# Kernel tuning notes

Hardware: AMD Instinct MI355X
Metric: run time of the kernel (lower is better)

## Reference

```python
import jax, jax.numpy as jnp
import numpy as np

DIM = 1024; HEADS = 8; DHEAD = 64; INNER = HEADS * DHEAD
WS = 512; B = 2; N = 2048; FF = 4 * DIM
NEG = -1e9


def layernorm(x, g, b, eps=1e-5):
    mu = jnp.mean(x, -1, keepdims=True)
    var = jnp.mean((x - mu) ** 2, -1, keepdims=True)
    return (x - mu) * jax.lax.rsqrt(var + eps) * g + b


def rmsnorm(x, g, eps=1e-6):
    return x * jax.lax.rsqrt(jnp.mean(x * x, -1, keepdims=True) + eps) * g


def rotate_half(x):
    x1, x2 = jnp.split(x, 2, -1)
    return jnp.concatenate([-x2, x1], -1)


def local_attention(q, k, v):
    # lucidrains LocalAttention: single-head over last dim, rotary pos emb,
    # window_size=WS, causal, look_backward=1, look_forward=0. n % WS == 0 so autopad no-op.
    b, n, d = q.shape
    w = n // WS
    inv_freq = 1.0 / (10000.0 ** (jnp.arange(0, d, 2, dtype=jnp.float32) / d))
    t = jnp.arange(n)
    freqs = t[:, None].astype(jnp.float32) * inv_freq[None, :]
    emb = jnp.concatenate([freqs, freqs], -1)           # [n, d]
    cos, sin = jnp.cos(emb), jnp.sin(emb)
    q = q * cos + rotate_half(q) * sin
    k = k * cos + rotate_half(k) * sin
    bq = q.reshape(b, w, WS, d) * (d ** -0.5)
    bk = k.reshape(b, w, WS, d)
    bv = v.reshape(b, w, WS, d)

    def look_around(x, pad_value):
        # gather current window + 1 window backward along the window axis
        pads = [(0, 0), (1, 0)] + [(0, 0)] * (x.ndim - 2)
        xp = jnp.pad(x, pads, constant_values=pad_value)
        return jnp.concatenate([xp[:, 0:w], xp[:, 1:w + 1]], axis=2)

    bk = look_around(bk, 0.0)                 # [b, w, 2*WS, d]
    bv = look_around(bv, 0.0)
    bt = t.reshape(w, WS)                     # query positions per window
    bqk = look_around(bt[None], -1)[0]        # key positions, pad = -1  [w, 2*WS]
    sim = jnp.einsum('bwie,bwje->bwij', bq, bk)  # [b, w, WS, 2*WS]
    mask = (bt[:, :, None] < bqk[:, None, :]) | (bqk[:, None, :] == -1)
    sim = jnp.where(mask[None], NEG, sim)
    attn = jax.nn.softmax(sim, -1)
    out = jnp.einsum('bwij,bwje->bwie', attn, bv)
    return out.reshape(b, n, d)


def setup_inputs() -> dict:
    key = jax.random.key(0)
    ks = jax.random.split(key, 10)
    s = 0.02
    f32 = jnp.float32
    return {
        'text': jax.random.normal(ks[0], (B, N, DIM), f32),
        'audio': jax.random.normal(ks[1], (B, N, DIM), f32),
        'video': jax.random.normal(ks[2], (B, N, DIM), f32),
        'Wa': jax.random.normal(ks[3], (DIM, DIM), f32) * s,
        'ba': jnp.zeros((DIM,), f32),
        'lna_g': jnp.ones((DIM,), f32), 'lna_b': jnp.zeros((DIM,), f32),
        'Wvid': jax.random.normal(ks[4], (DIM, DIM), f32) * s,
        'bvid': jnp.zeros((DIM,), f32),
        'lnv_g': jnp.ones((DIM,), f32), 'lnv_b': jnp.zeros((DIM,), f32),
        'ln1_g': jnp.ones((DIM,), f32), 'ln1_b': jnp.zeros((DIM,), f32),
        'Wq': jax.random.normal(ks[5], (DIM, INNER), f32) * s,
        'Wkv': jax.random.normal(ks[6], (DIM, 2 * INNER), f32) * s,
        'qn_g': jnp.ones((DHEAD,), f32), 'kn_g': jnp.ones((DHEAD,), f32),
        'Wo': jax.random.normal(ks[7], (INNER, DIM), f32) * s,
        'W1': jax.random.normal(ks[8], (DIM, FF), f32) * s,
        'b1': jnp.zeros((FF,), f32),
        'ln2_g': jnp.ones((FF,), f32), 'ln2_b': jnp.zeros((FF,), f32),
        'W2': jax.random.normal(ks[9], (FF, DIM), f32) * s,
        'b2': jnp.zeros((DIM,), f32),
    }


def reference(text, audio, video, Wa, ba, lna_g, lna_b, Wvid, bvid, lnv_g, lnv_b,
              ln1_g, ln1_b, Wq, Wkv, qn_g, kn_g, Wo, W1, b1, ln2_g, ln2_b, W2, b2):
    # modality -> text-token adapters (audio_to_text / video_to_text): linear + layernorm
    audio_t = layernorm(audio @ Wa + ba, lna_g, lna_b)
    video_t = layernorm(video @ Wvid + bvid, lnv_g, lnv_b)
    # windowed local attention: q=text, k=audio tokens, v=video tokens
    x = local_attention(text, audio_t, video_t)          # [B, N, DIM]
    # qk-norm full causal attention (flash=False: dense [B,H,N,N] scores)
    b, n, _ = x.shape
    h = layernorm(x, ln1_g, ln1_b)
    q = (h @ Wq).reshape(b, n, HEADS, DHEAD).transpose(0, 2, 1, 3)
    k, v = jnp.split(h @ Wkv, 2, -1)
    k = k.reshape(b, n, HEADS, DHEAD).transpose(0, 2, 1, 3)
    v = v.reshape(b, n, HEADS, DHEAD).transpose(0, 2, 1, 3)
    q = rmsnorm(q, qn_g)
    k = rmsnorm(k, kn_g)
    sim = jnp.einsum('bhid,bhjd->bhij', q, k) * (DHEAD ** -0.5)
    causal = jnp.tril(jnp.ones((n, n), bool))
    sim = jnp.where(causal[None, None], sim, NEG)
    attn = jax.nn.softmax(sim, -1)
    o = jnp.einsum('bhij,bhjd->bhid', attn, v).transpose(0, 2, 1, 3).reshape(b, n, INNER)
    x = o @ Wo
    x = x + x                                            # x = x + x in source
    # FFN: Linear -> GELU -> post-act LayerNorm -> Linear, + residual
    h1 = layernorm(jax.nn.gelu(x @ W1 + b1), ln2_g, ln2_b)
    return h1 @ W2 + b2 + x
```

## Files before the change

### kernel.cpp

```cpp
#include <hip/hip_runtime.h>
#include <hip/hip_bf16.h>

typedef __bf16 bf16;
typedef __bf16 bf16x8 __attribute__((ext_vector_type(8)));
typedef float  f32x4  __attribute__((ext_vector_type(4)));

static __device__ __forceinline__ float b2f(bf16 x) { return (float)x; }
static __device__ __forceinline__ bf16  f2b(float x) { return (bf16)x; }
static __device__ __forceinline__ float ldval(float v) { return v; }
static __device__ __forceinline__ float ldval(bf16 v)  { return (float)v; }

static __device__ __forceinline__ void gl_lds16(const bf16* g, bf16* l)
{
    __builtin_amdgcn_global_load_lds(
        (const __attribute__((address_space(1))) void*)g,
        (__attribute__((address_space(3))) void*)l,
        16, 0, 0);
}

__global__ void detect_dtype(const unsigned short* __restrict__ p, int* __restrict__ flag)
{
    if (threadIdx.x == 0 && blockIdx.x == 0) {
        int big = 0;
        for (int i = 0; i < 512; ++i) {
            int e = (p[i] >> 7) & 0xFF;
            if (e >= 0xE0) big++;
        }
        *flag = (big > 0) ? 1 : 0;
    }
}

__global__ __launch_bounds__(256) void convert2(
    const void* __restrict__ sa, const void* __restrict__ sb,
    bf16* __restrict__ da, bf16* __restrict__ db, int n,
    const int* __restrict__ flag)
{
    int f = *flag;
    int half = gridDim.x >> 1;
    const void* s = (blockIdx.x < half) ? sa : sb;
    bf16* d = (blockIdx.x < half) ? da : db;
    int bid = (blockIdx.x < half) ? blockIdx.x : blockIdx.x - half;
    for (int i = bid * 256 + threadIdx.x; i < n; i += half * 256) {
        float v = f ? ((const float*)s)[i] : (float)((const bf16*)s)[i];
        d[i] = f2b(v);
    }
}

struct VecPack { const void* src[14]; int n[14]; };
__global__ __launch_bounds__(256) void convert_vecs(
    VecPack vp, bf16* __restrict__ dst, const int* __restrict__ flag)
{
    int v = blockIdx.x;
    int f = *flag;
    const void* s = vp.src[v];
    int n = vp.n[v];
    bf16* d = dst + (size_t)v * 4096;
    for (int i = threadIdx.x; i < n; i += 256) {
        float x = f ? ((const float*)s)[i] : (float)((const bf16*)s)[i];
        d[i] = f2b(x);
    }
}

template <int EPI, int MT>
__global__ __launch_bounds__(256) void gemm_bt(
    const bf16* __restrict__ A0, int lda, int zsA, int zsA2,
    const bf16* __restrict__ B0, int ldb, int zsB, int zsB2,
    void* __restrict__ C0, int ldc, int zsC, int zsC2,
    const bf16* __restrict__ bias, int zsBias, float scale, int K)
{
    constexpr int IFR = MT / 32;
    __shared__ __align__(16) bf16 As[MT * 64];
    __shared__ __align__(16) bf16 Bs[128 * 64];
    const int z = blockIdx.z;
    const bf16* A  = A0 + (size_t)z * zsA + (size_t)(z >> 2) * zsA2;
    const bf16* Bt = B0 + (size_t)z * zsB + (size_t)(z >> 2) * zsB2;
    const size_t cbase = (size_t)z * zsC + (size_t)(z >> 2) * zsC2;
    if (bias) bias += (size_t)z * zsBias;
    const int tid  = threadIdx.x;
    const int lane = tid & 63, wave = tid >> 6;
    const int quad = lane >> 4, l16 = lane & 15;
    const size_t tm = (size_t)blockIdx.y * MT, tn = (size_t)blockIdx.x * 128;
    const int wm = (wave >> 1) * (MT / 2), wn = (wave & 1) * 64;
    const int srow = lane >> 3;
    const int scol = ((lane & 7) ^ srow) * 8;

    f32x4 acc[IFR][4];
    const f32x4 zro = {0.f, 0.f, 0.f, 0.f};
    #pragma unroll
    for (int i = 0; i < IFR; ++i)
        #pragma unroll
        for (int j = 0; j < 4; ++j) acc[i][j] = zro;

    const int swzA = l16 & 7;
    for (int k0 = 0; k0 < K; k0 += 64) {
        #pragma unroll
        for (int i = 0; i < IFR; ++i) {
            int chunk = (wave * IFR + i) * 64;
            int row = (chunk >> 3) + srow;
            gl_lds16(A + (tm + row) * (size_t)lda + k0 + scol, As + (size_t)chunk * 8);
        }
        #pragma unroll
        for (int i = 0; i < 4; ++i) {
            int chunk = (wave * 4 + i) * 64;
            int row = (chunk >> 3) + srow;
            gl_lds16(Bt + (tn + row) * (size_t)ldb + k0 + scol, Bs + (size_t)chunk * 8);
        }
        __syncthreads();
        #pragma unroll
        for (int kk = 0; kk < 2; ++kk) {
            bf16x8 af[IFR], bfr[4];
            #pragma unroll
            for (int i = 0; i < IFR; ++i) {
                int row = wm + i * 16 + l16;
                af[i] = *(const bf16x8*)(const void*)&As[(row * 8 + ((kk*4 + quad) ^ swzA)) * 8];
            }
            #pragma unroll
            for (int j = 0; j < 4; ++j) {
                int row = wn + j * 16 + l16;
                bfr[j] = *(const bf16x8*)(const void*)&Bs[(row * 8 + ((kk*4 + quad) ^ swzA)) * 8];
            }
            #pragma unroll
            for (int i = 0; i < IFR; ++i)
                #pragma unroll
                for (int j = 0; j < 4; ++j)
                    acc[i][j] = __builtin_amdgcn_mfma_f32_16x16x32_bf16(
                        af[i], bfr[j], acc[i][j], 0, 0, 0);
        }
        __syncthreads();
    }

    float* Cf = (float*)C0;
    bf16*  Cb = (bf16*)C0;
    #pragma unroll
    for (int i = 0; i < IFR; ++i) {
        #pragma unroll
        for (int j = 0; j < 4; ++j) {
            size_t col = tn + wn + j*16 + l16;
            float bb = bias ? b2f(bias[col]) : 0.f;
            #pragma unroll
            for (int r = 0; r < 4; ++r) {
                size_t row = tm + wm + i*16 + quad*4 + r;
                float v = acc[i][j][r] + bb;
                size_t off = cbase + row * (size_t)ldc + col;
                if (EPI == 0) {
                    Cf[off] = v;
                } else if (EPI == 1) {
                    Cb[off] = f2b(v * scale);
                } else {
                    float g = 0.5f * v * (1.f + tanhf(0.7978845608028654f *
                                  (v + 0.044715f * v * v * v)));
                    Cb[off] = f2b(g);
                }
            }
        }
    }
}

__global__ __launch_bounds__(512, 2) void gemm_ff1_8ph(
    const bf16* __restrict__ A, int lda,
    const bf16* __restrict__ Bt, int ldb,
    bf16* __restrict__ C, int ldc,
    const bf16* __restrict__ bias, int K)
{
    __shared__ __align__(16) bf16 As[2][256 * 64];
    __shared__ __align__(16) bf16 Bs[2][256 * 64];
    const int tid  = threadIdx.x;
    const int lane = tid & 63, wave = tid >> 6;
    const int quad = lane >> 4, l16 = lane & 15;
    const int wr = wave >> 2, wc = wave & 3;
    const size_t tm = (size_t)blockIdx.y * 256;
    const size_t tn = (size_t)blockIdx.x * 256;
    const int srow = lane >> 3;
    const int scol = ((lane & 7) ^ srow) * 8;
    const int swz  = l16 & 7;

    f32x4 acc[8][4];
    const f32x4 zro = {0.f, 0.f, 0.f, 0.f};
    #pragma unroll
    for (int m = 0; m < 8; ++m)
        #pragma unroll
        for (int n = 0; n < 4; ++n) acc[m][n] = zro;

    const bf16* aSrc[4];
    const bf16* bSrc[4];
    #pragma unroll
    for (int i = 0; i < 4; ++i) {
        int grow = wave * 32 + i * 8 + srow;
        aSrc[i] = A  + (tm + grow) * (size_t)lda + scol;
        bSrc[i] = Bt + (tn + grow) * (size_t)ldb + scol;
    }

#define STAGE(BUF, K0, I)                                                     \
    do {                                                                      \
        gl_lds16(aSrc[I] + (K0), &As[BUF][(wave * 4 + (I)) * 512]);           \
        gl_lds16(bSrc[I] + (K0), &Bs[BUF][(wave * 4 + (I)) * 512]);           \
    } while (0)

#define LDA_F(BUF, M, KK)                                                     \
    (*(const bf16x8*)(const void*)&As[BUF][(wr * 128 + (M) * 16 + l16) * 64 + \
        ((((KK) * 4 + quad) ^ swz) << 3)])
#define LDB_F(BUF, N, KK)                                                     \
    (*(const bf16x8*)(const void*)&Bs[BUF][(wc * 64 + (N) * 16 + l16) * 64 +  \
        ((((KK) * 4 + quad) ^ swz) << 3)])

#define PHASE(M0, M1, PREF_STMT, TAIL_STMT)                                   \
    {                                                                         \
        PREF_STMT;                                                            \
        bf16x8 x0 = LDA_F(cur, M0, 0), x1 = LDA_F(cur, M0, 1);                \
        bf16x8 y0 = LDA_F(cur, M1, 0), y1 = LDA_F(cur, M1, 1);                \
        asm volatile("s_barrier" ::: "memory");                               \
        __builtin_amdgcn_s_setprio(1);                                        \
        _Pragma("unroll")                                                     \
        for (int n = 0; n < 4; ++n) {                                         \
            acc[M0][n] = __builtin_amdgcn_mfma_f32_16x16x32_bf16(x0, bfr[n][0], acc[M0][n], 0, 0, 0); \
            acc[M0][n] = __builtin_amdgcn_mfma_f32_16x16x32_bf16(x1, bfr[n][1], acc[M0][n], 0, 0, 0); \
            acc[M1][n] = __builtin_amdgcn_mfma_f32_16x16x32_bf16(y0, bfr[n][0], acc[M1][n], 0, 0, 0); \
            acc[M1][n] = __builtin_amdgcn_mfma_f32_16x16x32_bf16(y1, bfr[n][1], acc[M1][n], 0, 0, 0); \
        }                                                                     \
        __builtin_amdgcn_s_setprio(0);                                        \
        TAIL_STMT;                                                            \
        asm volatile("s_barrier" ::: "memory");                               \
    }

    #pragma unroll
    for (int i = 0; i < 4; ++i) STAGE(0, 0, i);
    asm volatile("s_waitcnt vmcnt(0)" ::: "memory");
    asm volatile("s_barrier" ::: "memory");

    const int NT = K >> 6;
    bf16x8 bfr[4][2];
    for (int t = 0; t < NT; ++t) {
        const int cur = t & 1, nxt = cur ^ 1;
        const int k1  = (t + 1) << 6;
        const bool pref = (t + 1 < NT);

        #pragma unroll
        for (int n = 0; n < 4; ++n) {
            bfr[n][0] = LDB_F(cur, n, 0);
            bfr[n][1] = LDB_F(cur, n, 1);
        }
        PHASE(0, 1,
              if (pref) { STAGE(nxt, k1, 0); STAGE(nxt, k1, 1); }, )
        PHASE(2, 3,
              if (pref) { STAGE(nxt, k1, 2); STAGE(nxt, k1, 3); }, )
        PHASE(4, 5, , )
        PHASE(6, 7, ,
              asm volatile("s_waitcnt vmcnt(0)" ::: "memory"))
    }
#undef PHASE
#undef LDB_F
#undef LDA_F
#undef STAGE

    #pragma unroll
    for (int m = 0; m < 8; ++m) {
        #pragma unroll
        for (int n = 0; n < 4; ++n) {
            size_t col = tn + wc * 64 + n * 16 + l16;
            float bb = b2f(bias[col]);
            #pragma unroll
            for (int r = 0; r < 4; ++r) {
                size_t row = tm + wr * 128 + m * 16 + quad * 4 + r;
                float v = acc[m][n][r] + bb;
                float s = v * (1.5957691216057308f + 0.07135481627f * v * v);
                float g = v / (1.f + __expf(-s));
                C[row * (size_t)ldc + col] = f2b(g);
            }
        }
    }
}

__global__ void transpose_any(const void* __restrict__ in, int R, int C,
                              unsigned short* __restrict__ out, int ldo,
                              const int* __restrict__ flag)
{
    __shared__ unsigned short t[32][33];
    int f = *flag;
    int c0 = blockIdx.x * 32, r0 = blockIdx.y * 32;
    int tx = threadIdx.x, ty = threadIdx.y;
    for (int i = ty; i < 32; i += 8) {
        size_t idx = (size_t)(r0 + i) * C + c0 + tx;
        bf16 v = f ? f2b(((const float*)in)[idx]) : ((const bf16*)in)[idx];
        t[i][tx] = *(unsigned short*)&v;
    }
    __syncthreads();
    for (int i = ty; i < 32; i += 8)
        out[(size_t)(c0 + i) * ldo + r0 + tx] = t[tx][i];
}

__global__ void transpose_vt(const unsigned short* __restrict__ in,
                             unsigned short* __restrict__ out)
{
    __shared__ unsigned short t[32][33];
    int b = blockIdx.z;
    const unsigned short* src = in + (size_t)b * 2048 * 1024;
    unsigned short* dst = out + (size_t)b * 1024 * 2560;
    int c0 = blockIdx.x * 32, r0 = blockIdx.y * 32;
    int tx = threadIdx.x, ty = threadIdx.y;
    for (int i = ty; i < 32; i += 8)
        t[i][tx] = src[(size_t)(r0 + i) * 1024 + c0 + tx];
    __syncthreads();
    for (int i = ty; i < 32; i += 8)
        dst[(size_t)(c0 + i) * 2560 + 512 + r0 + tx] = t[tx][i];
}

__global__ void transpose_v(const float* __restrict__ qkv, bf16* __restrict__ Vt)
{
    __shared__ float t[32][33];
    int bh = blockIdx.z, b = bh >> 3, h = bh & 7;
    const float* src = qkv + (size_t)b * 2048 * 1536 + 1024 + h * 64;
    int c0 = blockIdx.x * 32, r0 = blockIdx.y * 32;
    int tx = threadIdx.x, ty = threadIdx.y;
    for (int i = ty; i < 32; i += 8)
        t[i][tx] = src[(size_t)(r0 + i) * 1536 + c0 + tx];
    __syncthreads();
    bf16* dst = Vt + (size_t)bh * 64 * 2048;
    for (int i = ty; i < 32; i += 8)
        dst[(size_t)(c0 + i) * 2048 + r0 + tx] = f2b(t[tx][i]);
}

template <typename Tin>
__global__ __launch_bounds__(256) void ln_rows(
    const Tin* __restrict__ in, int C,
    const bf16* __restrict__ g, const bf16* __restrict__ b,
    bf16* __restrict__ out, float eps)
{
    const int row = blockIdx.x, tid = threadIdx.x;
    const Tin* p = in + (size_t)row * C;
    float s = 0.f, ss = 0.f;
    for (int c = tid; c < C; c += 256) {
        float v = ldval(p[c]);
        s += v; ss += v * v;
    }
    #pragma unroll
    for (int d = 32; d > 0; d >>= 1) { s += __shfl_xor(s, d); ss += __shfl_xor(ss, d); }
    __shared__ float red[2][4];
    int wave = tid >> 6, lane = tid & 63;
    if (lane == 0) { red[0][wave] = s; red[1][wave] = ss; }
    __syncthreads();
    s  = red[0][0] + red[0][1] + red[0][2] + red[0][3];
    ss = red[1][0] + red[1][1] + red[1][2] + red[1][3];
    float mu   = s / C;
    float var  = ss / C - mu * mu;
    float rstd = rsqrtf(var + eps);
    bf16* q = out + (size_t)row * C;
    for (int c = tid; c < C; c += 256) {
        float v = ldval(p[c]);
        q[c] = f2b((v - mu) * rstd * b2f(g[c]) + b2f(b[c]));
    }
}

__global__ __launch_bounds__(256) void ln_rows2(
    const bf16* __restrict__ in,
    const bf16* __restrict__ g0, const bf16* __restrict__ b0,
    const bf16* __restrict__ g1, const bf16* __restrict__ b1,
    bf16* __restrict__ out0, bf16* __restrict__ out1)
{
    const int row = blockIdx.x, tid = threadIdx.x;
    const int sel = row >> 12;
    const bf16* p = in + (size_t)row * 1024;
    const bf16* g = sel ? g1 : g0;
    const bf16* b = sel ? b1 : b0;
    bf16* q = (sel ? out1 + (size_t)(row - 4096) * 1024 : out0 + (size_t)row * 1024);
    float s = 0.f, ss = 0.f;
    for (int c = tid; c < 1024; c += 256) {
        float v = b2f(p[c]);
        s += v; ss += v * v;
    }
    #pragma unroll
    for (int d = 32; d > 0; d >>= 1) { s += __shfl_xor(s, d); ss += __shfl_xor(ss, d); }
    __shared__ float red[2][4];
    int wave = tid >> 6, lane = tid & 63;
    if (lane == 0) { red[0][wave] = s; red[1][wave] = ss; }
    __syncthreads();
    s  = red[0][0] + red[0][1] + red[0][2] + red[0][3];
    ss = red[1][0] + red[1][1] + red[1][2] + red[1][3];
    float mu   = s * (1.f / 1024.f);
    float var  = ss * (1.f / 1024.f) - mu * mu;
    float rstd = rsqrtf(var + 1e-5f);
    for (int c = tid; c < 1024; c += 256) {
        float v = b2f(p[c]);
        q[c] = f2b((v - mu) * rstd * b2f(g[c]) + b2f(b[c]));
    }
}

__global__ __launch_bounds__(256) void rotary_kernel(
    const void* __restrict__ text, const int* __restrict__ flag,
    const bf16* __restrict__ audioT,
    bf16* __restrict__ qrot, bf16* __restrict__ krotPad)
{
    int row = blockIdx.x;
    int t = row & 2047, b = row >> 11;
    int tid = threadIdx.x;
    int f = *flag;
    const float lg = 9.210340371976184f / 512.f;
    size_t base = (size_t)row * 1024;
    size_t kb = ((size_t)(b * 2560 + 512 + t)) * 1024;
    for (int c = tid; c < 512; c += 256) {
        float invf = __expf(-(float)c * lg);
        float th = (float)t * invf;
        float sn, cs;
        sincosf(th, &sn, &cs);
        float q1 = f ? ((const float*)text)[base + c]
                     : b2f(((const bf16*)text)[base + c]);
        float q2 = f ? ((const float*)text)[base + c + 512]
                     : b2f(((const bf16*)text)[base + c + 512]);
        qrot[base + c]       = f2b((q1 * cs - q2 * sn) * 0.03125f);
        qrot[base + c + 512] = f2b((q2 * cs + q1 * sn) * 0.03125f);
        float k1 = b2f(audioT[base + c]), k2 = b2f(audioT[base + c + 512]);
        krotPad[kb + c]       = f2b(k1 * cs - k2 * sn);
        krotPad[kb + c + 512] = f2b(k2 * cs + k1 * sn);
    }
}

__global__ __launch_bounds__(256) void softmax_local(
    const float* __restrict__ sim, bf16* __restrict__ attn)
{
    int i  = blockIdx.x;
    int zz = blockIdx.y;
    int w  = zz & 3;
    int tid = threadIdx.x;
    const float* p = sim + ((size_t)zz * 512 + i) * 1024;
    bf16* q = attn + ((size_t)zz * 512 + i) * 1024;
    int jlo = (w == 0) ? 512 : 0;
    int jhi = 512 + i;
    float m = -1e30f;
    #pragma unroll
    for (int k = 0; k < 4; ++k) {
        int c = tid + k * 256;
        if (c >= jlo && c <= jhi) m = fmaxf(m, p[c]);
    }
    #pragma unroll
    for (int d = 32; d > 0; d >>= 1) m = fmaxf(m, __shfl_xor(m, d));
    __shared__ float red[2][4];
    int wave = tid >> 6, lane = tid & 63;
    if (lane == 0) red[0][wave] = m;
    __syncthreads();
    m = fmaxf(fmaxf(red[0][0], red[0][1]), fmaxf(red[0][2], red[0][3]));
    float pv[4];
    float s = 0.f;
    #pragma unroll
    for (int k = 0; k < 4; ++k) {
        int c = tid + k * 256;
        float e = (c >= jlo && c <= jhi) ? __expf(p[c] - m) : 0.f;
        pv[k] = e; s += e;
    }
    #pragma unroll
    for (int d = 32; d > 0; d >>= 1) s += __shfl_xor(s, d);
    if (lane == 0) red[1][wave] = s;
    __syncthreads();
    s = red[1][0] + red[1][1] + red[1][2] + red[1][3];
    float inv = 1.f / s;
    #pragma unroll
    for (int k = 0; k < 4; ++k) q[tid + k * 256] = f2b(pv[k] * inv);
}

__global__ __launch_bounds__(256) void pack_qk(
    const float* __restrict__ qkv, bf16* __restrict__ Qp, bf16* __restrict__ Kp,
    const bf16* __restrict__ qn_g, const bf16* __restrict__ kn_g)
{
    int gid  = blockIdx.x * 4 + (threadIdx.x >> 6);
    int lane = threadIdx.x & 63;
    int token = gid >> 4, r = gid & 15, part = r >> 3, h = r & 7;
    const float* p = qkv + (size_t)token * 1536 + part * 512 + h * 64 + lane;
    float v = *p;
    float ss = v * v;
    #pragma unroll
    for (int d = 32; d > 0; d >>= 1) ss += __shfl_xor(ss, d);
    float sc = rsqrtf(ss * (1.f / 64.f) + 1e-6f);
    const bf16* gw = part ? kn_g : qn_g;
    float outv = v * sc * b2f(gw[lane]);
    if (!part) outv *= 0.125f;
    int b = token >> 11, t = token & 2047;
    bf16* dst = (part ? Kp : Qp) + ((size_t)(b * 8 + h) * 2048 + t) * 64 + lane;
    *dst = f2b(outv);
}

__global__ __launch_bounds__(256) void flash_split(
    const bf16* __restrict__ Qp, const bf16* __restrict__ Kp,
    const bf16* __restrict__ Vt, bf16* __restrict__ o,
    float* __restrict__ Opart, float* __restrict__ MLpart)
{
    const int qb = blockIdx.x;
    const int chunk = blockIdx.y;
    const int nch = (qb >> 3) + 1;
    if (chunk >= nch) return;
    __shared__ __align__(16) bf16 Ks[64][72];
    __shared__ __align__(16) bf16 Vs[64][72];
    __shared__ __align__(16) bf16 Ps[4][16][72];
    const int bh = blockIdx.z, b = bh >> 3, h = bh & 7;
    const int qm = qb * 64;
    const int jt0 = chunk * 512;
    const int jt1 = min(jt0 + 512, qm + 64);
    const int tid = threadIdx.x, wave = tid >> 6, lane = tid & 63;
    const int quad = lane >> 4, l16 = lane & 15;
    const bf16* Qg = Qp + (size_t)bh * 2048 * 64;
    const bf16* Kg = Kp + (size_t)bh * 2048 * 64;
    const bf16* Vg = Vt + (size_t)bh * 64 * 2048;

    const int qrow = qm + wave * 16 + l16;
    bf16x8 qa[2];
    qa[0] = *(const bf16x8*)(const void*)(Qg + (size_t)qrow * 64 + quad * 8);
    qa[1] = *(const bf16x8*)(const void*)(Qg + (size_t)qrow * 64 + 32 + quad * 8);

    f32x4 oacc[4];
    const f32x4 zro = {0.f, 0.f, 0.f, 0.f};
    #pragma unroll
    for (int j = 0; j < 4; ++j) oacc[j] = zro;
    float mst[4] = {-1e30f, -1e30f, -1e30f, -1e30f};
    float lst[4] = {0.f, 0.f, 0.f, 0.f};

    const int ldr = tid >> 2, ldc = (tid & 3) * 16;
    for (int jt = jt0; jt < jt1; jt += 64) {
        *(uint4*)(void*)&Ks[ldr][ldc] =
            *(const uint4*)(const void*)(Kg + (size_t)(jt + ldr) * 64 + ldc);
        *(uint4*)(void*)&Ks[ldr][ldc + 8] =
            *(const uint4*)(const void*)(Kg + (size_t)(jt + ldr) * 64 + ldc + 8);
        *(uint4*)(void*)&Vs[ldr][ldc] =
            *(const uint4*)(const void*)(Vg + (size_t)ldr * 2048 + jt + ldc);
        *(uint4*)(void*)&Vs[ldr][ldc + 8] =
            *(const uint4*)(const void*)(Vg + (size_t)ldr * 2048 + jt + ldc + 8);
        __syncthreads();

        f32x4 s[4];
        #pragma unroll
        for (int j = 0; j < 4; ++j) s[j] = zro;
        #pragma unroll
        for (int kk = 0; kk < 2; ++kk) {
            #pragma unroll
            for (int j = 0; j < 4; ++j) {
                bf16x8 kb = *(const bf16x8*)(const void*)&Ks[j*16 + l16][kk*32 + quad*8];
                s[j] = __builtin_amdgcn_mfma_f32_16x16x32_bf16(qa[kk], kb, s[j], 0, 0, 0);
            }
        }

        if (jt + 63 > qm + wave * 16) {
            #pragma unroll
            for (int j = 0; j < 4; ++j) {
                int key = jt + j * 16 + l16;
                #pragma unroll
                for (int r = 0; r < 4; ++r) {
                    int row = qm + wave * 16 + quad * 4 + r;
                    if (key > row) s[j][r] = -1e30f;
                }
            }
        }

        f32x4 tmax = s[0];
        #pragma unroll
        for (int j = 1; j < 4; ++j)
            #pragma unroll
            for (int r = 0; r < 4; ++r) tmax[r] = fmaxf(tmax[r], s[j][r]);
        #pragma unroll
        for (int r = 0; r < 4; ++r) {
            float tv = tmax[r];
            #pragma unroll
            for (int d = 1; d < 16; d <<= 1) tv = fmaxf(tv, __shfl_xor(tv, d));
            tmax[r] = tv;
        }
        float scl[4];
        #pragma unroll
        for (int r = 0; r < 4; ++r) {
            float mn = fmaxf(mst[r], tmax[r]);
            scl[r] = __expf(mst[r] - mn);
            mst[r] = mn;
        }
        f32x4 psum = zro;
        #pragma unroll
        for (int j = 0; j < 4; ++j)
            #pragma unroll
            for (int r = 0; r < 4; ++r) {
                float e = __expf(s[j][r] - mst[r]);
                s[j][r] = e;
                psum[r] += e;
            }
        #pragma unroll
        for (int r = 0; r < 4; ++r) {
            float tv = psum[r];
            #pragma unroll
            for (int d = 1; d < 16; d <<= 1) tv += __shfl_xor(tv, d);
            lst[r] = lst[r] * scl[r] + tv;
        }
        #pragma unroll
        for (int j = 0; j < 4; ++j)
            #pragma unroll
            for (int r = 0; r < 4; ++r) oacc[j][r] *= scl[r];

        #pragma unroll
        for (int j = 0; j < 4; ++j)
            #pragma unroll
            for (int r = 0; r < 4; ++r)
                Ps[wave][quad*4 + r][j*16 + l16] = f2b(s[j][r]);
        bf16x8 pa[2];
        pa[0] = *(const bf16x8*)(const void*)&Ps[wave][l16][quad*8];
        pa[1] = *(const bf16x8*)(const void*)&Ps[wave][l16][32 + quad*8];

        #pragma unroll
        for (int kk = 0; kk < 2; ++kk) {
            #pragma unroll
            for (int j = 0; j < 4; ++j) {
                bf16x8 vb = *(const bf16x8*)(const void*)&Vs[j*16 + l16][kk*32 + quad*8];
                oacc[j] = __builtin_amdgcn_mfma_f32_16x16x32_bf16(pa[kk], vb, oacc[j], 0, 0, 0);
            }
        }
        __syncthreads();
    }

    if (nch == 1) {
        #pragma unroll
        for (int j = 0; j < 4; ++j) {
            #pragma unroll
            for (int r = 0; r < 4; ++r) {
                int t = qm + wave * 16 + quad * 4 + r;
                o[((size_t)(b * 2048 + t)) * 512 + h * 64 + j * 16 + l16] =
                    f2b(oacc[j][r] / lst[r]);
            }
        }
    } else {
        int pidx = (bh * 32 + qb) * 4 + chunk;
        float* Od = Opart + (size_t)pidx * 4096;
        #pragma unroll
        for (int j = 0; j < 4; ++j)
            #pragma unroll
            for (int r = 0; r < 4; ++r) {
                int row = wave * 16 + quad * 4 + r;
                Od[row * 64 + j * 16 + l16] = oacc[j][r];
            }
        if (l16 == 0) {
            #pragma unroll
            for (int r = 0; r < 4; ++r) {
                int row = wave * 16 + quad * 4 + r;
                MLpart[(size_t)pidx * 128 + row]      = mst[r];
                MLpart[(size_t)pidx * 128 + 64 + row] = lst[r];
            }
        }
    }
}

__global__ __launch_bounds__(256) void flash_combine(
    const float* __restrict__ Opart, const float* __restrict__ MLpart,
    bf16* __restrict__ o)
{
    int qb = blockIdx.x + 8;
    int bh = blockIdx.y, b = bh >> 3, h = bh & 7;
    int nch = (qb >> 3) + 1;
    int row = threadIdx.x >> 2;
    int d0 = (threadIdx.x & 3) * 16;
    int base = (bh * 32 + qb) * 4;
    float m[4], l[4], w[4];
    float mstar = -1e30f;
    for (int c = 0; c < nch; ++c) {
        m[c] = MLpart[(size_t)(base + c) * 128 + row];
        l[c] = MLpart[(size_t)(base + c) * 128 + 64 + row];
        mstar = fmaxf(mstar, m[c]);
    }
    float lstar = 0.f;
    for (int c = 0; c < nch; ++c) {
        w[c] = __expf(m[c] - mstar);
        lstar += l[c] * w[c];
    }
    float inv = 1.f / lstar;
    int t = qb * 64 + row;
    bf16* op = o + ((size_t)(b * 2048 + t)) * 512 + h * 64 + d0;
    #pragma unroll 4
    for (int dd = 0; dd < 16; ++dd) {
        float acc = 0.f;
        for (int c = 0; c < nch; ++c)
            acc += Opart[(size_t)(base + c) * 4096 + row * 64 + d0 + dd] * w[c];
        op[dd] = f2b(acc * inv);
    }
}

__global__ __launch_bounds__(256) void combine_ff2(
    const float* __restrict__ p0, const float* __restrict__ p1,
    const bf16* __restrict__ x2, const bf16* __restrict__ b2,
    float* __restrict__ out)
{
    int i4 = (blockIdx.x * 256 + threadIdx.x) * 4;
    #pragma unroll
    for (int k = 0; k < 4; ++k) {
        int i = i4 + k;
        out[i] = p0[i] + p1[i] + b2f(x2[i]) + b2f(b2[i & 1023]);
    }
}

static void launch_gemm(int epi, hipStream_t s,
                        const bf16* A, int lda, int zsA, int zsA2,
                        const bf16* Bt, int ldb, int zsB, int zsB2,
                        void* C, int ldc, int zsC, int zsC2,
                        const bf16* bias, int zsBias, float scale,
                        int M, int N, int K, int nz)
{
    bool mt64 = ((M >> 7) * (N >> 7) * nz) <= 512;
    dim3 blk(256);
    if (mt64) {
        dim3 g(N / 128, M / 64, nz);
        switch (epi) {
        case 0: gemm_bt<0,64><<<g, blk, 0, s>>>(A, lda, zsA, zsA2, Bt, ldb, zsB, zsB2, C, ldc, zsC, zsC2, bias, zsBias, scale, K); break;
        case 1: gemm_bt<1,64><<<g, blk, 0, s>>>(A, lda, zsA, zsA2, Bt, ldb, zsB, zsB2, C, ldc, zsC, zsC2, bias, zsBias, scale, K); break;
        default: gemm_bt<2,64><<<g, blk, 0, s>>>(A, lda, zsA, zsA2, Bt, ldb, zsB, zsB2, C, ldc, zsC, zsC2, bias, zsBias, scale, K); break;
        }
    } else {
        dim3 g(N / 128, M / 128, nz);
        switch (epi) {
        case 0: gemm_bt<0,128><<<g, blk, 0, s>>>(A, lda, zsA, zsA2, Bt, ldb, zsB, zsB2, C, ldc, zsC, zsC2, bias, zsBias, scale, K); break;
        case 1: gemm_bt<1,128><<<g, blk, 0, s>>>(A, lda, zsA, zsA2, Bt, ldb, zsB, zsB2, C, ldc, zsC, zsC2, bias, zsBias, scale, K); break;
        default: gemm_bt<2,128><<<g, blk, 0, s>>>(A, lda, zsA, zsA2, Bt, ldb, zsB, zsB2, C, ldc, zsC, zsC2, bias, zsBias, scale, K); break;
        }
    }
}

extern "C" void kernel_launch(void* const* d_in, const int* in_sizes, int n_in,
                              void* d_out, int out_size, void* d_ws, size_t ws_size,
                              hipStream_t stream)
{
    const void* text  = d_in[0];
    const void* audio = d_in[1];
    const void* video = d_in[2];
    const void* Wa    = d_in[3];
    const void* ba    = d_in[4];
    const void* lna_g = d_in[5];
    const void* lna_b = d_in[6];
    const void* Wvid  = d_in[7];
    const void* bvid  = d_in[8];
    const void* lnv_g = d_in[9];
    const void* lnv_b = d_in[10];
    const void* ln1_g = d_in[11];
    const void* ln1_b = d_in[12];
    const void* Wq    = d_in[13];
    const void* Wkv   = d_in[14];
    const void* qn_g  = d_in[15];
    const void* kn_g  = d_in[16];
    const void* Wo    = d_in[17];
    const void* W1    = d_in[18];
    const void* b1    = d_in[19];
    const void* ln2_g = d_in[20];
    const void* ln2_b = d_in[21];
    const void* W2    = d_in[22];
    const void* b2    = d_in[23];

    char* ws = (char*)d_ws;
    size_t off = 0;
    auto alloc = [&](size_t bytes) -> char* {
        char* p = ws + off;
        off += (bytes + 255) & ~(size_t)255;
        return p;
    };
    const size_t MB = 1024 * 1024;
    int*  flag  = (int*)alloc(256);
    bf16* vecs  = (bf16*)alloc(14 * 4096 * 2);
    bf16* WqkvT = (bf16*)alloc((size_t)1536 * 1024 * 2);
    bf16* WoT   = (bf16*)alloc((size_t)1024 * 512 * 2);
    bf16* W1T   = (bf16*)alloc((size_t)4096 * 1024 * 2);
    bf16* W2T   = (bf16*)alloc((size_t)1024 * 4096 * 2);
    char* regionIn = alloc(24 * MB);
    char* region2  = alloc(32 * MB);
    char* regionH  = alloc(8 * MB);
    char* regionX  = alloc(8 * MB);
    char* regionO  = alloc(4 * MB);
    bf16* qrot    = (bf16*)alloc((size_t)4096 * 1024 * 2);
    bf16* krotPad = (bf16*)alloc((size_t)2 * 2560 * 1024 * 2);
    bf16* VTpad   = (bf16*)alloc((size_t)2 * 1024 * 2560 * 2);
    bf16* attn    = (bf16*)alloc((size_t)8 * 512 * 1024 * 2);

    bf16*  audioC = (bf16*)regionIn;
    bf16*  videoC = audioC + (size_t)4096 * 1024;
    float* qkvF   = (float*)regionIn;
    bf16*  tmp2   = (bf16*)region2;
    float* tmpF   = (float*)region2;
    float* xF     = (float*)(region2 + 16 * MB);
    bf16*  g      = (bf16*)region2;
    bf16*  audioT = (bf16*)regionH;
    bf16*  h      = (bf16*)regionH;
    bf16*  videoT = (bf16*)regionX;
    bf16*  x2     = (bf16*)regionX;
    bf16*  WaT    = (bf16*)regionO;
    bf16*  WvT    = WaT + (size_t)1024 * 1024;
    bf16*  o      = (bf16*)regionO;
    bf16*  Qp     = qrot;
    bf16*  Kp     = krotPad;
    bf16*  Vth    = attn;
    float* Opart  = (float*)regionIn;
    float* MLpart = Opart + (size_t)16 * 32 * 4 * 4096;
    float* p0     = (float*)regionIn;
    float* p1     = (float*)VTpad;

    bf16* baC   = vecs + 0 * 4096;
    bf16* bvidC = vecs + 1 * 4096;
    bf16* lnagC = vecs + 2 * 4096;
    bf16* lnabC = vecs + 3 * 4096;
    bf16* lnvgC = vecs + 4 * 4096;
    bf16* lnvbC = vecs + 5 * 4096;
    bf16* ln1gC = vecs + 6 * 4096;
    bf16* ln1bC = vecs + 7 * 4096;
    bf16* qngC  = vecs + 8 * 4096;
    bf16* kngC  = vecs + 9 * 4096;
    bf16* b1C   = vecs + 10 * 4096;
    bf16* ln2gC = vecs + 11 * 4096;
    bf16* ln2bC = vecs + 12 * 4096;
    bf16* b2C   = vecs + 13 * 4096;

    detect_dtype<<<1, 64, 0, stream>>>((const unsigned short*)text, flag);

    const int NTOK = 4096 * 1024;
    convert2<<<4096, 256, 0, stream>>>(audio, video, audioC, videoC, NTOK, flag);
    VecPack vp;
    const void* vsrc[14] = {ba, bvid, lna_g, lna_b, lnv_g, lnv_b, ln1_g, ln1_b,
                            qn_g, kn_g, b1, ln2_g, ln2_b, b2};
    int vn[14] = {1024, 1024, 1024, 1024, 1024, 1024, 1024, 1024,
                  64, 64, 4096, 4096, 4096, 1024};
    for (int i = 0; i < 14; ++i) { vp.src[i] = vsrc[i]; vp.n[i] = vn[i]; }
    convert_vecs<<<14, 256, 0, stream>>>(vp, vecs, flag);

    dim3 tb(32, 8);
    transpose_any<<<dim3(32, 32), tb, 0, stream>>>(Wa, 1024, 1024, (unsigned short*)WaT, 1024, flag);
    transpose_any<<<dim3(32, 32), tb, 0, stream>>>(Wvid, 1024, 1024, (unsigned short*)WvT, 1024, flag);
    transpose_any<<<dim3(16, 32), tb, 0, stream>>>(Wq, 1024, 512, (unsigned short*)WqkvT, 1024, flag);
    transpose_any<<<dim3(32, 32), tb, 0, stream>>>(Wkv, 1024, 1024, (unsigned short*)(WqkvT + (size_t)512 * 1024), 1024, flag);
    transpose_any<<<dim3(32, 16), tb, 0, stream>>>(Wo, 512, 1024, (unsigned short*)WoT, 512, flag);
    transpose_any<<<dim3(128, 32), tb, 0, stream>>>(W1, 1024, 4096, (unsigned short*)W1T, 1024, flag);
    transpose_any<<<dim3(32, 128), tb, 0, stream>>>(W2, 4096, 1024, (unsigned short*)W2T, 4096, flag);

    launch_gemm(1, stream, audioC, 1024, 4096*1024, 0, WaT, 1024, 1024*1024, 0,
                tmp2, 1024, 4096*1024, 0, baC, 4096, 1.f, 4096, 1024, 1024, 2);
    ln_rows2<<<8192, 256, 0, stream>>>(tmp2, lnagC, lnabC, lnvgC, lnvbC, audioT, videoT);

    hipMemsetAsync(krotPad, 0, (size_t)2 * 2560 * 1024 * 2, stream);
    hipMemsetAsync(VTpad, 0, (size_t)2 * 1024 * 2560 * 2, stream);
    rotary_kernel<<<4096, 256, 0, stream>>>(text, flag, audioT, qrot, krotPad);
    transpose_vt<<<dim3(32, 64, 2), tb, 0, stream>>>(
        (const unsigned short*)videoT, (unsigned short*)VTpad);

    launch_gemm(0, stream, qrot, 1024, 512*1024, 0,
                krotPad, 1024, 512*1024, 512*1024,
                tmpF, 1024, 512*1024, 0, nullptr, 0, 1.f, 512, 1024, 1024, 8);
    softmax_local<<<dim3(512, 8), 256, 0, stream>>>(tmpF, attn);
    launch_gemm(0, stream, attn, 1024, 512*1024, 0,
                VTpad, 2560, 512, 1024*2560 - 2048,
                xF, 1024, 512*1024, 0, nullptr, 0, 1.f, 512, 1024, 1024, 8);

    ln_rows<float><<<4096, 256, 0, stream>>>(xF, 1024, ln1gC, ln1bC, h, 1e-5f);
    launch_gemm(0, stream, h, 1024, 0, 0, WqkvT, 1024, 0, 0,
                qkvF, 1536, 0, 0, nullptr, 0, 1.f, 4096, 1536, 1024, 1);
    pack_qk<<<16384, 256, 0, stream>>>(qkvF, Qp, Kp, qngC, kngC);
    transpose_v<<<dim3(2, 64, 16), tb, 0, stream>>>(qkvF, Vth);
    flash_split<<<dim3(32, 4, 16), 256, 0, stream>>>(Qp, Kp, Vth, o, Opart, MLpart);
    flash_combine<<<dim3(24, 16), 256, 0, stream>>>(Opart, MLpart, o);

    launch_gemm(1, stream, o, 512, 0, 0, WoT, 512, 0, 0,
                x2, 1024, 0, 0, nullptr, 0, 2.f, 4096, 1024, 512, 1);
    gemm_ff1_8ph<<<dim3(16, 16), 512, 0, stream>>>(x2, 1024, W1T, 1024,
                                                   g, 4096, b1C, 1024);
    ln_rows<bf16><<<4096, 256, 0, stream>>>(g, 4096, ln2gC, ln2bC, g, 1e-5f);
    launch_gemm(0, stream, g, 4096, 2048, 0, W2T, 4096, 2048, 0,
                p0, 1024, (int)(p1 - p0), 0, nullptr, 0, 1.f, 4096, 1024, 2048, 2);
    combine_ff2<<<4096, 256, 0, stream>>>(p0, p1, x2, b2C, (float*)d_out);

    (void)in_sizes; (void)n_in; (void)out_size; (void)ws_size;
}
```

Baseline: 612.7 us.

## Fuse split-KV flash attention into single pass with double-buffered K/V prefetch

Replaces the split-KV flash attention plus combine kernel with one kernel per query block that walks all causal key tiles. Global loads for the next K/V tile are issued into registers before the current tile's MFMAs and stored into a second LDS buffer, so there is one barrier per tile. Heaviest query blocks are scheduled first. This removes the partial-output traffic and the extra combine launch, but drops parallelism to 512 blocks with a long causal tail, and doubles LDS use per block.

```diff
diff --git a/kernel.cpp b/kernel.cpp
--- a/kernel.cpp
+++ b/kernel.cpp
@@ -476,22 +476,16 @@
     *dst = f2b(outv);
 }
 
-__global__ __launch_bounds__(256) void flash_split(
+__global__ __launch_bounds__(256) void flash_fused(
     const bf16* __restrict__ Qp, const bf16* __restrict__ Kp,
-    const bf16* __restrict__ Vt, bf16* __restrict__ o,
-    float* __restrict__ Opart, float* __restrict__ MLpart)
-{
-    const int qb = blockIdx.x;
-    const int chunk = blockIdx.y;
-    const int nch = (qb >> 3) + 1;
-    if (chunk >= nch) return;
-    __shared__ __align__(16) bf16 Ks[64][72];
-    __shared__ __align__(16) bf16 Vs[64][72];
+    const bf16* __restrict__ Vt, bf16* __restrict__ o)
+{
+    __shared__ __align__(16) bf16 Ks[2][64][72];
+    __shared__ __align__(16) bf16 Vs[2][64][72];
     __shared__ __align__(16) bf16 Ps[4][16][72];
-    const int bh = blockIdx.z, b = bh >> 3, h = bh & 7;
+    const int qb = 31 - blockIdx.x;
+    const int bh = blockIdx.y, b = bh >> 3, h = bh & 7;
     const int qm = qb * 64;
-    const int jt0 = chunk * 512;
-    const int jt1 = min(jt0 + 512, qm + 64);
     const int tid = threadIdx.x, wave = tid >> 6, lane = tid & 63;
     const int quad = lane >> 4, l16 = lane & 15;
     const bf16* Qg = Qp + (size_t)bh * 2048 * 64;
@@ -511,16 +505,31 @@
     float lst[4] = {0.f, 0.f, 0.f, 0.f};
 
     const int ldr = tid >> 2, ldc = (tid & 3) * 16;
-    for (int jt = jt0; jt < jt1; jt += 64) {
-        *(uint4*)(void*)&Ks[ldr][ldc] =
-            *(const uint4*)(const void*)(Kg + (size_t)(jt + ldr) * 64 + ldc);
-        *(uint4*)(void*)&Ks[ldr][ldc + 8] =
-            *(const uint4*)(const void*)(Kg + (size_t)(jt + ldr) * 64 + ldc + 8);
-        *(uint4*)(void*)&Vs[ldr][ldc] =
-            *(const uint4*)(const void*)(Vg + (size_t)ldr * 2048 + jt + ldc);
-        *(uint4*)(void*)&Vs[ldr][ldc + 8] =
-            *(const uint4*)(const void*)(Vg + (size_t)ldr * 2048 + jt + ldc + 8);
-        __syncthreads();
+    {
+        uint4 ka = *(const uint4*)(const void*)(Kg + (size_t)ldr * 64 + ldc);
+        uint4 kb = *(const uint4*)(const void*)(Kg + (size_t)ldr * 64 + ldc + 8);
+        uint4 va = *(const uint4*)(const void*)(Vg + (size_t)ldr * 2048 + ldc);
+        uint4 vb = *(const uint4*)(const void*)(Vg + (size_t)ldr * 2048 + ldc + 8);
+        *(uint4*)(void*)&Ks[0][ldr][ldc]     = ka;
+        *(uint4*)(void*)&Ks[0][ldr][ldc + 8] = kb;
+        *(uint4*)(void*)&Vs[0][ldr][ldc]     = va;
+        *(uint4*)(void*)&Vs[0][ldr][ldc + 8] = vb;
+    }
+    __syncthreads();
+
+    const int ntiles = qb + 1;
+    for (int t = 0; t < ntiles; ++t) {
+        const int cur = t & 1, nxt = cur ^ 1;
+        const int jt = t * 64;
+        const bool pref = (t + 1 < ntiles);
+        uint4 ka, kb, va, vb;
+        if (pref) {
+            int jn = jt + 64;
+            ka = *(const uint4*)(const void*)(Kg + (size_t)(jn + ldr) * 64 + ldc);
+            kb = *(const uint4*)(const void*)(Kg + (size_t)(jn + ldr) * 64 + ldc + 8);
+            va = *(const uint4*)(const void*)(Vg + (size_t)ldr * 2048 + jn + ldc);
+            vb = *(const uint4*)(const void*)(Vg + (size_t)ldr * 2048 + jn + ldc + 8);
+        }
 
         f32x4 s[4];
         #pragma unroll
@@ -529,8 +538,8 @@
         for (int kk = 0; kk < 2; ++kk) {
             #pragma unroll
             for (int j = 0; j < 4; ++j) {
-                bf16x8 kb = *(const bf16x8*)(const void*)&Ks[j*16 + l16][kk*32 + quad*8];
-                s[j] = __builtin_amdgcn_mfma_f32_16x16x32_bf16(qa[kk], kb, s[j], 0, 0, 0);
+                bf16x8 kf = *(const bf16x8*)(const void*)&Ks[cur][j*16 + l16][kk*32 + quad*8];
+                s[j] = __builtin_amdgcn_mfma_f32_16x16x32_bf16(qa[kk], kf, s[j], 0, 0, 0);
             }
         }
 
@@ -599,75 +608,28 @@
         for (int kk = 0; kk < 2; ++kk) {
             #pragma unroll
             for (int j = 0; j < 4; ++j) {
-                bf16x8 vb = *(const bf16x8*)(const void*)&Vs[j*16 + l16][kk*32 + quad*8];
-                oacc[j] = __builtin_amdgcn_mfma_f32_16x16x32_bf16(pa[kk], vb, oacc[j], 0, 0, 0);
+                bf16x8 vf = *(const bf16x8*)(const void*)&Vs[cur][j*16 + l16][kk*32 + quad*8];
+                oacc[j] = __builtin_amdgcn_mfma_f32_16x16x32_bf16(pa[kk], vf, oacc[j], 0, 0, 0);
             }
         }
-        __syncthreads();
-    }
-
-    if (nch == 1) {
-        #pragma unroll
-        for (int j = 0; j < 4; ++j) {
-            #pragma unroll
-            for (int r = 0; r < 4; ++r) {
-                int t = qm + wave * 16 + quad * 4 + r;
-                o[((size_t)(b * 2048 + t)) * 512 + h * 64 + j * 16 + l16] =
-                    f2b(oacc[j][r] / lst[r]);
-            }
-        }
-    } else {
-        int pidx = (bh * 32 + qb) * 4 + chunk;
-        float* Od = Opart + (size_t)pidx * 4096;
-        #pragma unroll
-        for (int j = 0; j < 4; ++j)
-            #pragma unroll
-            for (int r = 0; r < 4; ++r) {
-                int row = wave * 16 + quad * 4 + r;
-                Od[row * 64 + j * 16 + l16] = oacc[j][r];
-            }
-        if (l16 == 0) {
-            #pragma unroll
-            for (int r = 0; r < 4; ++r) {
-                int row = wave * 16 + quad * 4 + r;
-                MLpart[(size_t)pidx * 128 + row]      = mst[r];
-                MLpart[(size_t)pidx * 128 + 64 + row] = lst[r];
-            }
-        }
-    }
-}
-
-__global__ __launch_bounds__(256) void flash_combine(
-    const float* __restrict__ Opart, const float* __restrict__ MLpart,
-    bf16* __restrict__ o)
-{
-    int qb = blockIdx.x + 8;
-    int bh = blockIdx.y, b = bh >> 3, h = bh & 7;
-    int nch = (qb >> 3) + 1;
-    int row = threadIdx.x >> 2;
-    int d0 = (threadIdx.x & 3) * 16;
-    int base = (bh * 32 + qb) * 4;
-    float m[4], l[4], w[4];
-    float mstar = -1e30f;
-    for (int c = 0; c < nch; ++c) {
-        m[c] = MLpart[(size_t)(base + c) * 128 + row];
-        l[c] = MLpart[(size_t)(base + c) * 128 + 64 + row];
-        mstar = fmaxf(mstar, m[c]);
-    }
-    float lstar = 0.f;
-    for (int c = 0; c < nch; ++c) {
-        w[c] = __expf(m[c] - mstar);
-        lstar += l[c] * w[c];
-    }
-    float inv = 1.f / lstar;
-    int t = qb * 64 + row;
-    bf16* op = o + ((size_t)(b * 2048 + t)) * 512 + h * 64 + d0;
-    #pragma unroll 4
-    for (int dd = 0; dd < 16; ++dd) {
-        float acc = 0.f;
-        for (int c = 0; c < nch; ++c)
-            acc += Opart[(size_t)(base + c) * 4096 + row * 64 + d0 + dd] * w[c];
-        op[dd] = f2b(acc * inv);
+
+        if (pref) {
+            *(uint4*)(void*)&Ks[nxt][ldr][ldc]     = ka;
+            *(uint4*)(void*)&Ks[nxt][ldr][ldc + 8] = kb;
+            *(uint4*)(void*)&Vs[nxt][ldr][ldc]     = va;
+            *(uint4*)(void*)&Vs[nxt][ldr][ldc + 8] = vb;
+            __syncthreads();
+        }
+    }
+
+    #pragma unroll
+    for (int j = 0; j < 4; ++j) {
+        #pragma unroll
+        for (int r = 0; r < 4; ++r) {
+            int t = qm + wave * 16 + quad * 4 + r;
+            o[((size_t)(b * 2048 + t)) * 512 + h * 64 + j * 16 + l16] =
+                f2b(oacc[j][r] / lst[r]);
+        }
     }
 }
 
@@ -780,8 +742,6 @@
     bf16*  Qp     = qrot;
     bf16*  Kp     = krotPad;
     bf16*  Vth    = attn;
-    float* Opart  = (float*)regionIn;
-    float* MLpart = Opart + (size_t)16 * 32 * 4 * 4096;
     float* p0     = (float*)regionIn;
     float* p1     = (float*)VTpad;
 
@@ -844,8 +804,7 @@
                 qkvF, 1536, 0, 0, nullptr, 0, 1.f, 4096, 1536, 1024, 1);
     pack_qk<<<16384, 256, 0, stream>>>(qkvF, Qp, Kp, qngC, kngC);
     transpose_v<<<dim3(2, 64, 16), tb, 0, stream>>>(qkvF, Vth);
-    flash_split<<<dim3(32, 4, 16), 256, 0, stream>>>(Qp, Kp, Vth, o, Opart, MLpart);
-    flash_combine<<<dim3(24, 16), 256, 0, stream>>>(Opart, MLpart, o);
+    flash_fused<<<dim3(32, 16), 256, 0, stream>>>(Qp, Kp, Vth, o);
 
     launch_gemm(1, stream, o, 512, 0, 0, WoT, 512, 0, 0,
                 x2, 1024, 0, 0, nullptr, 0, 2.f, 4096, 1024, 512, 1);
```

Result: faster. 578.6 us (-5.6%).
